# Kernel tuning notes

Hardware: AMD Instinct MI355X
Metric: run time of the kernel (lower is better)

The kernel has to match this reference:

```python
import jax, jax.numpy as jnp
import numpy as np
import math

B, H, W, DM = 4, 64, 64, 96
DS, DCONV, EXPAND = 16, 3, 2
DI = EXPAND * DM
DTR = math.ceil(DM / 16)
K = 4
HID = 4 * DI


def layernorm(x, g, b, eps=1e-5):
    m = x.mean(-1, keepdims=True)
    v = ((x - m) ** 2).mean(-1, keepdims=True)
    return (x - m) / jnp.sqrt(v + eps) * g + b


def dwconv(x, w, b=None):
    # x: (B,C,H,W), w: (C,1,kh,kw) depthwise, odd kernel => SAME padding == k//2
    out = jax.lax.conv_general_dilated(x, w, (1, 1), 'SAME',
                                       feature_group_count=x.shape[1],
                                       dimension_numbers=('NCHW', 'OIHW', 'NCHW'))
    if b is not None:
        out = out + b[None, :, None, None]
    return out


def ss2d_core(xc, x_proj_w, dt_projs_w, dt_projs_b, A_logs, Ds):
    # xc: (b, d_inner, h, w) -> (b, d_inner, L) summed over 4 scan directions
    b, c, h, w = xc.shape
    L = h * w
    x_hw = xc.reshape(b, c, L)
    x_wh = xc.transpose(0, 1, 3, 2).reshape(b, c, L)
    xs = jnp.stack([x_hw, x_wh], axis=1)                 # (b,2,c,L)
    xs = jnp.concatenate([xs, jnp.flip(xs, -1)], axis=1)  # (b,4,c,L)
    x_dbl = jnp.einsum('bkdl,kcd->bkcl', xs, x_proj_w)
    dts, Bs, Cs = jnp.split(x_dbl, [DTR, DTR + DS], axis=2)
    dts = jnp.einsum('bkrl,kdr->bkdl', dts, dt_projs_w)
    delta = jax.nn.softplus(dts + dt_projs_b[None, :, :, None])  # (b,K,c,L)
    A = -jnp.exp(A_logs).reshape(K, c, DS)                       # (K,c,n)

    def step(hst, inp):
        x_t, d_t, B_t, C_t = inp  # (b,K,c),(b,K,c),(b,K,n),(b,K,n)
        dA = jnp.exp(d_t[..., None] * A)                       # (b,K,c,n)
        hst = hst * dA + (d_t * x_t)[..., None] * B_t[:, :, None, :]
        y = jnp.einsum('bkdn,bkn->bkd', hst, C_t)
        return hst, y

    seq = (jnp.moveaxis(xs, -1, 0), jnp.moveaxis(delta, -1, 0),
           jnp.moveaxis(Bs, -1, 0), jnp.moveaxis(Cs, -1, 0))
    h0 = jnp.zeros((b, K, c, DS), xc.dtype)
    _, ys = jax.lax.scan(step, h0, seq)          # (L,b,K,c)
    ys = jnp.moveaxis(ys, 0, -1)                 # (b,K,c,L)
    ys = ys + Ds.reshape(K, c)[None, :, :, None] * xs
    y1 = ys[:, 0]
    inv = jnp.flip(ys[:, 2:4], -1)
    y2 = inv[:, 0]
    wh = ys[:, 1].reshape(b, c, w, h).swapaxes(2, 3).reshape(b, c, L)
    invwh = inv[:, 1].reshape(b, c, w, h).swapaxes(2, 3).reshape(b, c, L)
    return y1 + y2 + wh + invwh


def msffn(y, in_w, in_b, dw1, dw3, dw5, ln_g, ln_b, out_w, out_b):
    hcl = jax.nn.silu(y @ in_w.T + in_b)          # (b,h,w,HID)
    hc = hcl.transpose(0, 3, 1, 2)
    hc = hc + dwconv(hc, dw1) + dwconv(hc, dw3) + dwconv(hc, dw5)
    hn = layernorm(hc.transpose(0, 2, 3, 1), ln_g, ln_b)
    return hn @ out_w.T + out_b


def setup_inputs() -> dict:
    key = jax.random.key(0)
    ks = jax.random.split(key, 16)
    dt_init_std = DTR ** -0.5
    dt = jnp.exp(jax.random.uniform(ks[0], (K, DI)) * (math.log(0.1) - math.log(0.001)) + math.log(0.001))
    dt = jnp.clip(dt, 1e-4, None)
    inv_dt = dt + jnp.log(-jnp.expm1(-dt))          # softplus-inverse init for dt bias
    A_logs = jnp.tile(jnp.log(jnp.arange(1, DS + 1, dtype=jnp.float32))[None, :], (K * DI, 1))
    r = lambda i, sh, s: jax.random.normal(ks[i], sh, jnp.float32) * s
    return {
        'x': r(1, (B, H, W, DM), 1.0),
        'in_proj_w': r(2, (2 * DI, DM), DM ** -0.5),
        'conv_w': r(3, (DI, 1, DCONV, DCONV), 0.2),
        'conv_b': jnp.zeros((DI,), jnp.float32),
        'x_proj_w': r(4, (K, DTR + 2 * DS, DI), DI ** -0.5),
        'dt_projs_w': jax.random.uniform(ks[5], (K, DI, DTR), minval=-dt_init_std, maxval=dt_init_std),
        'dt_projs_b': inv_dt,
        'A_logs': A_logs,
        'Ds': jnp.ones((K * DI,), jnp.float32),
        'out_norm_g': jnp.ones((DI,), jnp.float32),
        'out_norm_b': jnp.zeros((DI,), jnp.float32),
        'out_proj_w': r(6, (DM, DI), DI ** -0.5),
        'ffn_in_w': r(7, (HID, DI), DI ** -0.5),
        'ffn_in_b': jnp.zeros((HID,), jnp.float32),
        'ffn_dw1': r(8, (HID, 1, 1, 1), 0.3),
        'ffn_dw3': r(9, (HID, 1, 3, 3), 0.2),
        'ffn_dw5': r(10, (HID, 1, 5, 5), 0.1),
        'ffn_ln_g': jnp.ones((HID,), jnp.float32),
        'ffn_ln_b': jnp.zeros((HID,), jnp.float32),
        'ffn_out_w': r(11, (DM, HID), HID ** -0.5),
        'ffn_out_b': jnp.zeros((DM,), jnp.float32),
        'skip_scale': jnp.ones((1,), jnp.float32),
    }


def reference(x, in_proj_w, conv_w, conv_b, x_proj_w, dt_projs_w, dt_projs_b, A_logs, Ds,
              out_norm_g, out_norm_b, out_proj_w, ffn_in_w, ffn_in_b, ffn_dw1, ffn_dw3,
              ffn_dw5, ffn_ln_g, ffn_ln_b, ffn_out_w, ffn_out_b, skip_scale):
    b, h, w, _ = x.shape
    xz = x @ in_proj_w.T                          # (b,h,w,2*DI)
    xi, z = jnp.split(xz, 2, axis=-1)
    xc = jax.nn.silu(dwconv(xi.transpose(0, 3, 1, 2), conv_w, conv_b))  # (b,DI,h,w)
    y = ss2d_core(xc, x_proj_w, dt_projs_w, dt_projs_b, A_logs, Ds)     # (b,DI,L)
    y = y.swapaxes(1, 2).reshape(b, h, w, DI)
    y = layernorm(y, out_norm_g, out_norm_b)
    y = y * jax.nn.silu(z)
    out = y @ out_proj_w.T
    ffn = msffn(y, ffn_in_w, ffn_in_b, ffn_dw1, ffn_dw3, ffn_dw5,
                ffn_ln_g, ffn_ln_b, ffn_out_w, ffn_out_b)
    return out + skip_scale * ffn
```

## Files before the change

### kernel.cpp

```cpp
#include <hip/hip_runtime.h>
#include <hip/hip_bf16.h>

constexpr int BB = 4, HH = 64, WW = 64, DMv = 96;
constexpr int DSn = 16, DIv = 192, DTRv = 6, KKv = 4, HIDv = 768;
constexpr int LL = 4096;
constexpr int NC = 64, CHK = LL / NC;
constexpr int NR = BB * LL;
constexpr int XDS = 40;

constexpr size_t S_xi   = (size_t)BB * LL * DIv;
constexpr size_t S_xdbl = (size_t)BB * KKv * LL * XDS;
constexpr size_t S_big  = (size_t)BB * KKv * LL * DIv;
constexpr size_t S_sp   = (size_t)BB * KKv * NC * DIv * DSn;

typedef __attribute__((ext_vector_type(8))) short short8;
typedef __attribute__((ext_vector_type(4))) short short4v;
typedef __attribute__((ext_vector_type(4))) float floatx4;

__device__ __forceinline__ float sigf(float x) { return 1.f / (1.f + __expf(-x)); }
__device__ __forceinline__ float softp(float x) {
  return (x > 20.f) ? x : __logf(1.f + __expf(x));
}
__device__ __forceinline__ short bfbits(float v) {
  __hip_bfloat16 h = __float2bfloat16(v);
  return *(short*)&h;
}

__device__ __forceinline__ int lmap(int k, int l) {
  int lr = (k & 2) ? (LL - 1 - l) : l;
  return (k & 1) ? (((lr & 63) << 6) | (lr >> 6)) : lr;
}

__global__ void k_wprep(const float* __restrict__ fiw, const float* __restrict__ opw,
                        const float* __restrict__ fow, const float* __restrict__ in_w,
                        const float* __restrict__ xpw, const float* __restrict__ x,
                        float* __restrict__ wt, float* __restrict__ xt,
                        short* __restrict__ fiwP, short* __restrict__ opwP,
                        short* __restrict__ fowP, short* __restrict__ wcatP) {
  int bx = blockIdx.x, t = threadIdx.x;
  __shared__ float smbuf[32 * 65];
  if (bx < 36) {
    int r0 = (bx / 3) * 32, c0 = (bx % 3) * 32;
    float (*tile)[33] = (float(*)[33])smbuf;
    int tc = t & 31, tr = t >> 5;
#pragma unroll
    for (int i = 0; i < 4; ++i)
      tile[tr + i * 8][tc] = in_w[(size_t)(r0 + tr + i * 8) * 96 + c0 + tc];
    __syncthreads();
#pragma unroll
    for (int i = 0; i < 4; ++i)
      wt[(size_t)(c0 + tr + i * 8) * 384 + r0 + tc] = tile[tc][tr + i * 8];
    return;
  }
  if (bx < 804) {
    int i4 = bx - 36;
    int r0 = (i4 / 3) * 64, k0 = (i4 % 3) * 32;
    float (*tile)[65] = (float(*)[65])smbuf;
#pragma unroll
    for (int ii = 0; ii < 8; ++ii) {
      int i = (t >> 5) + ii * 8, j = t & 31;
      tile[j][i] = x[(size_t)(r0 + i) * 96 + k0 + j];
    }
    __syncthreads();
#pragma unroll
    for (int jj = 0; jj < 8; ++jj) {
      int j = (t >> 6) + jj * 4, i = t & 63;
      xt[(size_t)(k0 + j) * NR + r0 + i] = tile[j][i];
    }
    return;
  }
  int lane = t & 63, ln16 = lane & 15, qd = lane >> 4;
  if (bx < 876) {
    int f = (bx - 804) * 4 + (t >> 6);
    int kt = f / 48, ntg = f % 48;
    int n = ntg * 16 + ln16;
#pragma unroll
    for (int j = 0; j < 8; ++j) {
      int k = kt * 32 + qd * 8 + j;
      fiwP[(size_t)f * 512 + lane * 8 + j] = bfbits(fiw[(size_t)n * DIv + k]);
    }
    return;
  }
  if (bx < 894) {
    int u = (bx - 876) * 4 + (t >> 6);
    int f = u >> 1, part = u & 1;
    int kt = f / 6, ntg = f % 6;
    int n = ntg * 16 + ln16;
#pragma unroll
    for (int j = 0; j < 8; ++j) {
      int k = kt * 32 + qd * 8 + j;
      float w = opw[(size_t)n * DIv + k];
      __hip_bfloat16 h = __float2bfloat16(w);
      float v = part ? (w - (float)h) : w;
      opwP[((size_t)(part * 36 + f)) * 512 + lane * 8 + j] = bfbits(v);
    }
    return;
  }
  if (bx < 966) {
    int u = (bx - 894) * 4 + (t >> 6);
    int f = u >> 1, part = u & 1;
    int kt = f / 6, ntg = f % 6;
    int n = ntg * 16 + ln16;
#pragma unroll
    for (int j = 0; j < 8; ++j) {
      int k = kt * 32 + qd * 8 + j;
      float w = fow[(size_t)n * HIDv + k];
      __hip_bfloat16 h = __float2bfloat16(w);
      float v = part ? (w - (float)h) : w;
      fowP[((size_t)(part * 144 + f)) * 512 + lane * 8 + j] = bfbits(v);
    }
    return;
  }
  {
    int u = (bx - 966) * 4 + (t >> 6);
    int p = u / 60, r = u % 60;
    int part = r / 30, r2 = r % 30;
    int kt = r2 / 5, g = r2 % 5;
    int n = g * 16 + ln16;
#pragma unroll
    for (int j = 0; j < 8; ++j) {
      int kd = kt * 32 + qd * 8 + j;
      float w = 0.f;
      if (n < 76) {
        int ksel = ((n >= 38) ? 2 : 0) + p;
        int cc = (n >= 38) ? n - 38 : n;
        w = xpw[(size_t)(ksel * 38 + cc) * DIv + kd];
      }
      __hip_bfloat16 h = __float2bfloat16(w);
      float v = part ? (w - (float)h) : w;
      wcatP[((size_t)(((p * 2 + part) * 6 + kt) * 5 + g)) * 512 + lane * 8 + j] = bfbits(v);
    }
  }
}

__global__ void k_inproj(const float* __restrict__ xt, const float* __restrict__ wt,
                         float* __restrict__ xi, float* __restrict__ z) {
  int t = threadIdx.x;
  int wv = t >> 6, lane = t & 63;
  int rq = blockIdx.x * 256 + wv * 64 + lane;
  int c0 = blockIdx.y * 8;
  const float4* xt4 = (const float4*)xt;
  float4 acc[8];
#pragma unroll
  for (int c = 0; c < 8; ++c) acc[c] = make_float4(0.f, 0.f, 0.f, 0.f);
  for (int k = 0; k < 96; ++k) {
    float4 xv = xt4[(size_t)k * (NR / 4) + rq];
    const float* wr = wt + k * 384 + c0;
#pragma unroll
    for (int c = 0; c < 8; ++c) {
      float w = wr[c];
      acc[c].x += w * xv.x; acc[c].y += w * xv.y;
      acc[c].z += w * xv.z; acc[c].w += w * xv.w;
    }
  }
  float* dst; int cc;
  if (c0 < DIv) { dst = xi; cc = c0; } else { dst = z; cc = c0 - DIv; }
#pragma unroll
  for (int li = 0; li < 4; ++li) {
    size_t row = (size_t)rq * 4 + li;
    float4 v0, v1;
    v0.x = (&acc[0].x)[li]; v0.y = (&acc[1].x)[li];
    v0.z = (&acc[2].x)[li]; v0.w = (&acc[3].x)[li];
    v1.x = (&acc[4].x)[li]; v1.y = (&acc[5].x)[li];
    v1.z = (&acc[6].x)[li]; v1.w = (&acc[7].x)[li];
    float4* o4 = (float4*)(dst + row * DIv + cc);
    o4[0] = v0; o4[1] = v1;
  }
}

constexpr int TW2 = 18;
__global__ void k_dwconv3(const float* __restrict__ xi, const float* __restrict__ cw,
                          const float* __restrict__ cb, float* __restrict__ xc,
                          short* __restrict__ xcBh, short* __restrict__ xcBl) {
  int tile = blockIdx.x;
  int cg = blockIdx.y, b = blockIdx.z;
  int t = threadIdx.x;
  int ti0 = (tile >> 2) * 16, tj0 = (tile & 3) * 16;
  __shared__ float sm[TW2 * TW2 * 32];

  for (int e = t; e < TW2 * TW2 * 32; e += 256) {
    int ec = e & 31;
    int sp = e >> 5;
    int hi = sp / TW2, hj = sp % TW2;
    int gi = ti0 + hi - 1, gj = tj0 + hj - 1;
    float v = 0.f;
    if ((unsigned)gi < (unsigned)HH && (unsigned)gj < (unsigned)WW)
      v = xi[((size_t)b * LL + gi * WW + gj) * DIv + cg * 32 + ec];
    sm[e] = v;
  }

  int c = t & 31, s0 = t >> 5;
  int cglob = cg * 32 + c;
  float wc[9];
#pragma unroll
  for (int j = 0; j < 9; ++j) wc[j] = cw[cglob * 9 + j];
  float bv = cb[cglob];
  __syncthreads();

  float res[32];
  for (int i = 0; i < 32; ++i) {
    int p = s0 + (i << 3);
    int r = p >> 4, q = p & 15;
    float s = bv;
#pragma unroll
    for (int di = 0; di < 3; ++di)
#pragma unroll
      for (int dj = 0; dj < 3; ++dj)
        s += sm[((r + di) * TW2 + (q + dj)) * 32 + c] * wc[di * 3 + dj];
    res[i] = s * sigf(s);
  }
  __syncthreads();
  for (int i = 0; i < 32; ++i) {
    int p = s0 + (i << 3);
    sm[p * 35 + c] = res[i];
  }
  __syncthreads();
  for (int it = 0; it < 32; ++it) {
    int e = it * 256 + t;
    int p = e >> 5, ec = e & 31;
    int l = (ti0 + (p >> 4)) * WW + tj0 + (p & 15);
    float v = sm[p * 35 + ec];
    size_t idx = ((size_t)b * LL + l) * DIv + cg * 32 + ec;
    xc[idx] = v;
    __hip_bfloat16 hh = __float2bfloat16(v);
    xcBh[idx] = *(short*)&hh;
    xcBl[idx] = bfbits(v - (float)hh);
  }
}

__global__ void k_xdblmf(const short* __restrict__ xcBh, const short* __restrict__ xcBl,
                         const short* __restrict__ wcatP, float* __restrict__ xdbl) {
  int t = threadIdx.x;
  int wv = t >> 6, lane = t & 63;
  int ln16 = lane & 15, qd = lane >> 4;
  int pb = blockIdx.y;
  int p = pb >> 2, b = pb & 3;
  int m0 = blockIdx.x * 64 + wv * 16;
  int r = m0 + ln16;
  int l = p ? (((r & 63) << 6) | (r >> 6)) : r;
  const short* ah = xcBh + ((size_t)(b * LL + l)) * DIv + qd * 8;
  const short* al = xcBl + ((size_t)(b * LL + l)) * DIv + qd * 8;
  floatx4 acc[5];
  floatx4 zero4 = {0.f, 0.f, 0.f, 0.f};
#pragma unroll
  for (int g = 0; g < 5; ++g) acc[g] = zero4;
#pragma unroll
  for (int kt = 0; kt < 6; ++kt) {
    short8 Ah = *(const short8*)(ah + kt * 32);
    short8 Al = *(const short8*)(al + kt * 32);
    const short* bh = wcatP + ((size_t)(((p * 2 + 0) * 6 + kt) * 5)) * 512 + lane * 8;
    const short* bl = wcatP + ((size_t)(((p * 2 + 1) * 6 + kt) * 5)) * 512 + lane * 8;
#pragma unroll
    for (int g = 0; g < 5; ++g) {
      short8 Bh = *(const short8*)(bh + (size_t)g * 512);
      short8 Bl = *(const short8*)(bl + (size_t)g * 512);
      acc[g] = __builtin_amdgcn_mfma_f32_16x16x32_bf16(Ah, Bh, acc[g], 0, 0, 0);
      acc[g] = __builtin_amdgcn_mfma_f32_16x16x32_bf16(Al, Bh, acc[g], 0, 0, 0);
      acc[g] = __builtin_amdgcn_mfma_f32_16x16x32_bf16(Ah, Bl, acc[g], 0, 0, 0);
    }
  }
#pragma unroll
  for (int g = 0; g < 5; ++g) {
    int col = g * 16 + ln16;
    if (col < 76) {
#pragma unroll
      for (int rr = 0; rr < 4; ++rr) {
        int rowr = m0 + qd * 4 + rr;
        int kk = (col >= 38) ? (2 + p) : p;
        int cc = (col >= 38) ? col - 38 : col;
        int lpos = (col >= 38) ? (LL - 1 - rowr) : rowr;
        int phys = cc + (cc >= 6 ? 2 : 0);
        size_t ro = (((size_t)(b * KKv + kk)) * LL + lpos) * XDS;
        xdbl[ro + phys] = acc[g][rr];
        if (col == 5) { xdbl[ro + 6] = 0.f; xdbl[ro + 7] = 0.f; }
      }
    }
  }
}

__global__ void k_scan1(const float* __restrict__ xdbl, const float* __restrict__ xc,
                        const float* __restrict__ alogs, const float* __restrict__ dtw,
                        const float* __restrict__ dtb,
                        float* __restrict__ S, float* __restrict__ P) {
  int bx = blockIdx.x;
  int c = bx / 3, dblk = bx % 3;
  int k = blockIdx.y, b = blockIdx.z;
  int t = threadIdx.x, dl = t >> 2, nq = t & 3;
  int d = dblk * 64 + dl;
  __shared__ float de_s[16][64], xv_s[16][64], bc_s[16][16];
  float A[4];
#pragma unroll
  for (int j = 0; j < 4; ++j)
    A[j] = -__expf(alogs[(size_t)(k * DIv + d) * DSn + nq * 4 + j]);
  int derow = t >> 4, dec0 = (t & 15) * 4;
  float DTW[4][6], DTB[4];
#pragma unroll
  for (int jj = 0; jj < 4; ++jj) {
    int dd = k * DIv + dblk * 64 + dec0 + jj;
    DTB[jj] = dtb[dd];
#pragma unroll
    for (int r2 = 0; r2 < 6; ++r2) DTW[jj][r2] = dtw[(size_t)dd * 6 + r2];
  }
  size_t bkL = (size_t)(b * KKv + k) * LL;
  const float* xq = xdbl + bkL * XDS;
  const float* xcb = xc + (size_t)b * LL * DIv;
  float h[4] = {0.f, 0.f, 0.f, 0.f}, sA[4] = {0.f, 0.f, 0.f, 0.f};
  int l0 = c * CHK;
  for (int tile = 0; tile < CHK / 16; ++tile) {
    int lt = l0 + tile * 16;
    __syncthreads();
    {
      int r = t >> 4, q = t & 15;
      int lc = lmap(k, lt + r);
      *(float4*)&xv_s[r][q * 4] = *(const float4*)(xcb + (size_t)lc * DIv + dblk * 64 + q * 4);
      if (t < 64) {
        int r2 = t >> 2, q2 = t & 3;
        *(float4*)&bc_s[r2][q2 * 4] = *(const float4*)(xq + (size_t)(lt + r2) * XDS + 8 + q2 * 4);
      }
      const float* dtp = xq + (size_t)(lt + derow) * XDS;
      float d0 = dtp[0], d1 = dtp[1], d2 = dtp[2], d3 = dtp[3], d4 = dtp[4], d5 = dtp[5];
#pragma unroll
      for (int jj = 0; jj < 4; ++jj) {
        float s = DTB[jj] + d0 * DTW[jj][0] + d1 * DTW[jj][1] + d2 * DTW[jj][2]
                          + d3 * DTW[jj][3] + d4 * DTW[jj][4] + d5 * DTW[jj][5];
        de_s[derow][dec0 + jj] = softp(s);
      }
    }
    __syncthreads();
#pragma unroll
    for (int i2 = 0; i2 < 16; ++i2) {
      float de = de_s[i2][dl];
      float xv = xv_s[i2][dl];
      float4 Bv = *(float4*)&bc_s[i2][nq * 4];
      float db = de * xv;
#pragma unroll
      for (int j = 0; j < 4; ++j) {
        float u = de * A[j];
        sA[j] += u;
        h[j] = h[j] * __expf(u) + db * (&Bv.x)[j];
      }
    }
  }
  size_t o = ((((size_t)(b * KKv + k) * NC + c) * 3 + dblk) * 1024) + (size_t)t * 4;
  float4 hs, ps;
#pragma unroll
  for (int j = 0; j < 4; ++j) { (&hs.x)[j] = h[j]; (&ps.x)[j] = __expf(sA[j]); }
  *(float4*)(S + o) = hs;
  *(float4*)(P + o) = ps;
}

__global__ void k_scan2(float* __restrict__ S, const float* __restrict__ P) {
  int dblk = blockIdx.x, k = blockIdx.y, b = blockIdx.z;
  int t = threadIdx.x;
  size_t base = (((size_t)(b * KKv + k) * NC) * 3 + dblk) * 1024 + (size_t)t * 4;
  float4 h = make_float4(0.f, 0.f, 0.f, 0.f);
  for (int c = 0; c < NC; ++c) {
    size_t o = base + (size_t)c * 3 * 1024;
    float4 s = *(float4*)(S + o), p = *(float4*)(P + o);
    *(float4*)(S + o) = h;
    h.x = s.x + p.x * h.x; h.y = s.y + p.y * h.y;
    h.z = s.z + p.z * h.z; h.w = s.w + p.w * h.w;
  }
}

__global__ void k_scan3(const float* __restrict__ xdbl, const float* __restrict__ xc,
                        const float* __restrict__ alogs, const float* __restrict__ dtw,
                        const float* __restrict__ dtb,
                        const float* __restrict__ Hin, float* __restrict__ ys) {
  int bx = blockIdx.x;
  int c = bx / 3, dblk = bx % 3;
  int k = blockIdx.y, b = blockIdx.z;
  int t = threadIdx.x, dl = t >> 2, nq = t & 3;
  int d = dblk * 64 + dl;
  __shared__ float de_s[16][64], xv_s[16][64], bc_s[16][32];
  float A[4];
#pragma unroll
  for (int j = 0; j < 4; ++j)
    A[j] = -__expf(alogs[(size_t)(k * DIv + d) * DSn + nq * 4 + j]);
  int derow = t >> 4, dec0 = (t & 15) * 4;
  float DTW[4][6], DTB[4];
#pragma unroll
  for (int jj = 0; jj < 4; ++jj) {
    int dd = k * DIv + dblk * 64 + dec0 + jj;
    DTB[jj] = dtb[dd];
#pragma unroll
    for (int r2 = 0; r2 < 6; ++r2) DTW[jj][r2] = dtw[(size_t)dd * 6 + r2];
  }
  size_t bkL = (size_t)(b * KKv + k) * LL;
  const float* xq = xdbl + bkL * XDS;
  const float* xcb = xc + (size_t)b * LL * DIv;
  float* yp = ys + bkL * DIv + d;
  size_t o = ((((size_t)(b * KKv + k) * NC + c) * 3 + dblk) * 1024) + (size_t)t * 4;
  float4 h4 = *(const float4*)(Hin + o);
  float h[4] = {h4.x, h4.y, h4.z, h4.w};
  int l0 = c * CHK;
  for (int tile = 0; tile < CHK / 16; ++tile) {
    int lt = l0 + tile * 16;
    __syncthreads();
    {
      int r = t >> 4, q = t & 15;
      int lc = lmap(k, lt + r);
      *(float4*)&xv_s[r][q * 4] = *(const float4*)(xcb + (size_t)lc * DIv + dblk * 64 + q * 4);
      if (t < 128) {
        int r2 = t >> 3, q2 = t & 7;
        *(float4*)&bc_s[r2][q2 * 4] = *(const float4*)(xq + (size_t)(lt + r2) * XDS + 8 + q2 * 4);
      }
      const float* dtp = xq + (size_t)(lt + derow) * XDS;
      float d0 = dtp[0], d1 = dtp[1], d2 = dtp[2], d3 = dtp[3], d4 = dtp[4], d5 = dtp[5];
#pragma unroll
      for (int jj = 0; jj < 4; ++jj) {
        float s = DTB[jj] + d0 * DTW[jj][0] + d1 * DTW[jj][1] + d2 * DTW[jj][2]
                          + d3 * DTW[jj][3] + d4 * DTW[jj][4] + d5 * DTW[jj][5];
        de_s[derow][dec0 + jj] = softp(s);
      }
    }
    __syncthreads();
#pragma unroll
    for (int i2 = 0; i2 < 16; ++i2) {
      float de = de_s[i2][dl];
      float xv = xv_s[i2][dl];
      float4 Bv = *(float4*)&bc_s[i2][nq * 4];
      float4 Cv = *(float4*)&bc_s[i2][16 + nq * 4];
      float db = de * xv;
      float p = 0.f;
#pragma unroll
      for (int j = 0; j < 4; ++j) {
        h[j] = h[j] * __expf(de * A[j]) + db * (&Bv.x)[j];
        p += h[j] * (&Cv.x)[j];
      }
      p += __shfl_down(p, 2, 4);
      p += __shfl_down(p, 1, 4);
      if (nq == 0) yp[(size_t)(lt + i2) * DIv] = p;
    }
  }
}

__global__ void k_comlnt(const float* __restrict__ ys, const float* __restrict__ xc,
                         const float* __restrict__ Ds, const float* __restrict__ z,
                         const float* __restrict__ g, const float* __restrict__ be,
                         __hip_bfloat16* __restrict__ ygtB,
                         __hip_bfloat16* __restrict__ ygtBl) {
  int bl0 = blockIdx.x * 8;
  int b = bl0 >> 12, l0 = bl0 & 4095;
  int t = threadIdx.x;
  __shared__ float vbuf[8 * 193];
  __shared__ float m_[8], rs_[8];
  {
    int li = t >> 5, lane32 = t & 31;
    size_t base = (size_t)b * KKv * LL * DIv;
    int l = l0 + li;
    int lT = ((l & 63) << 6) | (l >> 6);
    const float* r0 = ys + base + (size_t)l * DIv;
    const float* r2 = ys + base + ((size_t)2 * LL + (LL - 1 - l)) * DIv;
    const float* r1 = ys + base + ((size_t)1 * LL + lT) * DIv;
    const float* r3 = ys + base + ((size_t)3 * LL + (LL - 1 - lT)) * DIv;
    const float* xr = xc + ((size_t)b * LL + l) * DIv;
#pragma unroll
    for (int cc = 0; cc < 6; ++cc) {
      int d = lane32 + cc * 32;
      float sd = Ds[d] + Ds[DIv + d] + Ds[2 * DIv + d] + Ds[3 * DIv + d];
      vbuf[li * 193 + d] = r0[d] + r2[d] + r1[d] + r3[d] + sd * xr[d];
    }
  }
  __syncthreads();
  {
    int r = t >> 5, q = t & 31;
    float s = 0.f, qq = 0.f;
#pragma unroll
    for (int j = 0; j < 6; ++j) {
      float v = vbuf[r * 193 + q + j * 32];
      s += v; qq += v * v;
    }
    s += __shfl_down(s, 16, 32); qq += __shfl_down(qq, 16, 32);
    s += __shfl_down(s, 8, 32);  qq += __shfl_down(qq, 8, 32);
    s += __shfl_down(s, 4, 32);  qq += __shfl_down(qq, 4, 32);
    s += __shfl_down(s, 2, 32);  qq += __shfl_down(qq, 2, 32);
    s += __shfl_down(s, 1, 32);  qq += __shfl_down(qq, 1, 32);
    if (q == 0) {
      float m = s / DIv;
      m_[r] = m;
      rs_[r] = rsqrtf(qq / DIv - m * m + 1e-5f);
    }
  }
  __syncthreads();
  int tc = t & 31, tr = t >> 5;
#pragma unroll
  for (int ch = 0; ch < 6; ++ch) {
    int c0 = ch * 32;
    float gg = g[c0 + tc], bb = be[c0 + tc];
    float v = vbuf[tr * 193 + c0 + tc];
    float zz = z[(size_t)(bl0 + tr) * DIv + c0 + tc];
    float val = (v - m_[tr]) * rs_[tr] * gg + bb;
    float gated = val * zz * sigf(zz);
    __hip_bfloat16 h = __float2bfloat16(gated);
    ygtB[(size_t)(bl0 + tr) * DIv + c0 + tc] = h;
    ygtBl[(size_t)(bl0 + tr) * DIv + c0 + tc] = __float2bfloat16(gated - (float)h);
  }
}

__global__ void k_ffnmf(const __hip_bfloat16* __restrict__ ygtB,
                        const short* __restrict__ fiwP,
                        const float* __restrict__ bias, float* __restrict__ hcl) {
  int t = threadIdx.x;
  int wv = t >> 6, lane = t & 63;
  int ln16 = lane & 15, qd = lane >> 4;
  int m0 = blockIdx.x * 64 + wv * 16;
  int n0 = blockIdx.y * 64;
  int ntg0 = n0 >> 4;
  floatx4 acc[4];
  floatx4 zero4 = {0.f, 0.f, 0.f, 0.f};
#pragma unroll
  for (int nt = 0; nt < 4; ++nt) acc[nt] = zero4;
  const short* arow = (const short*)ygtB + (size_t)(m0 + ln16) * DIv + qd * 8;
#pragma unroll
  for (int kt = 0; kt < 6; ++kt) {
    short8 a = *(const short8*)(arow + kt * 32);
    const short* bb = fiwP + ((size_t)(kt * 48 + ntg0) * 64 + lane) * 8;
#pragma unroll
    for (int nt = 0; nt < 4; ++nt) {
      short8 bfr = *(const short8*)(bb + (size_t)nt * 512);
      acc[nt] = __builtin_amdgcn_mfma_f32_16x16x32_bf16(a, bfr, acc[nt], 0, 0, 0);
    }
  }
#pragma unroll
  for (int nt = 0; nt < 4; ++nt) {
    int col = n0 + nt * 16 + ln16;
    float bv = bias[col];
#pragma unroll
    for (int r = 0; r < 4; ++r) {
      int row = m0 + qd * 4 + r;
      float s = acc[nt][r] + bv;
      hcl[(size_t)row * HIDv + col] = s * sigf(s);
    }
  }
}

constexpr int TS = 16, CG = 16, TW = TS + 4;
__global__ void k_ffnconv2(const float* __restrict__ hcl, const float* __restrict__ w1,
                           const float* __restrict__ w3, const float* __restrict__ w5,
                           float* __restrict__ hc2) {
  int tile = blockIdx.x;
  int cg = blockIdx.y, b = blockIdx.z;
  int t = threadIdx.x;
  int ti0 = (tile >> 2) * TS, tj0 = (tile & 3) * TS;
  __shared__ float sm[TW * TW * CG];

  for (int e = t; e < TW * TW * CG; e += 256) {
    int ec = e & 15;
    int sp = e >> 4;
    int hi = sp / TW, hj = sp % TW;
    int gi = ti0 + hi - 2, gj = tj0 + hj - 2;
    float v = 0.f;
    if ((unsigned)gi < (unsigned)HH && (unsigned)gj < (unsigned)WW)
      v = hcl[((size_t)b * LL + gi * WW + gj) * HIDv + cg * CG + ec];
    sm[e] = v;
  }

  int c = t & 15;
  int q = t >> 4;
  int cglob = cg * CG + c;
  float wc[25];
#pragma unroll
  for (int di = 0; di < 5; ++di)
#pragma unroll
    for (int dj = 0; dj < 5; ++dj) {
      float w = w5[cglob * 25 + di * 5 + dj];
      if (di >= 1 && di <= 3 && dj >= 1 && dj <= 3)
        w += w3[cglob * 9 + (di - 1) * 3 + (dj - 1)];
      if (di == 2 && dj == 2) w += 1.f + w1[cglob];
      wc[di * 5 + dj] = w;
    }
  __syncthreads();

  float win[5][5];
#pragma unroll
  for (int di = 0; di < 4; ++di)
#pragma unroll
    for (int dj = 0; dj < 5; ++dj)
      win[di][dj] = sm[(di * TW + (q + dj)) * CG + c];
#pragma unroll
  for (int r = 0; r < 16; ++r) {
    int slot = (r + 4) % 5;
#pragma unroll
    for (int dj = 0; dj < 5; ++dj)
      win[slot][dj] = sm[(((r + 4) * TW) + (q + dj)) * CG + c];
    float s = 0.f;
#pragma unroll
    for (int di = 0; di < 5; ++di) {
      int wsl = (r + di) % 5;
#pragma unroll
      for (int dj = 0; dj < 5; ++dj)
        s += win[wsl][dj] * wc[di * 5 + dj];
    }
    hc2[((size_t)b * LL + (ti0 + r) * WW + (tj0 + q)) * HIDv + cglob] = s;
  }
}

constexpr int LNROWS = 8, LNPAD = 776;
__global__ void k_ln2b(const float* __restrict__ hc2, const float* __restrict__ g,
                       const float* __restrict__ be,
                       short* __restrict__ hnBh, short* __restrict__ hnBl) {
  int r0 = blockIdx.x * LNROWS;
  int t = threadIdx.x;
  __shared__ float rows[LNROWS * LNPAD];
  __shared__ float m_[LNROWS], rs_[LNROWS];
#pragma unroll
  for (int i = 0; i < 6; ++i) {
    int idx4 = t + i * 256;
    int row = idx4 / 192, c4 = idx4 % 192;
    float4 v = *(const float4*)(hc2 + (size_t)(r0 + row) * HIDv + c4 * 4);
    *(float4*)&rows[row * LNPAD + c4 * 4] = v;
  }
  __syncthreads();
  {
    int r = t >> 5, q = t & 31;
    float s = 0.f, qq = 0.f;
#pragma unroll
    for (int j = 0; j < 24; ++j) {
      float v = rows[r * LNPAD + q + j * 32];
      s += v; qq += v * v;
    }
    s += __shfl_down(s, 16, 32); qq += __shfl_down(qq, 16, 32);
    s += __shfl_down(s, 8, 32);  qq += __shfl_down(qq, 8, 32);
    s += __shfl_down(s, 4, 32);  qq += __shfl_down(qq, 4, 32);
    s += __shfl_down(s, 2, 32);  qq += __shfl_down(qq, 2, 32);
    s += __shfl_down(s, 1, 32);  qq += __shfl_down(qq, 1, 32);
    if (q == 0) {
      float m = s / HIDv;
      m_[r] = m;
      rs_[r] = rsqrtf(qq / HIDv - m * m + 1e-5f);
    }
  }
  __syncthreads();
#pragma unroll
  for (int i = 0; i < 6; ++i) {
    int idx4 = t + i * 256;
    int row = idx4 / 192, c4 = idx4 % 192;
    float4 v = *(const float4*)&rows[row * LNPAD + c4 * 4];
    float4 gv = *(const float4*)(g + c4 * 4);
    float4 bv = *(const float4*)(be + c4 * 4);
    float m = m_[row], rs = rs_[row];
    short4v hh, ll;
#pragma unroll
    for (int j = 0; j < 4; ++j) {
      float val = ((&v.x)[j] - m) * rs * (&gv.x)[j] + (&bv.x)[j];
      __hip_bfloat16 h = __float2bfloat16(val);
      hh[j] = *(short*)&h;
      ll[j] = bfbits(val - (float)h);
    }
    size_t o = (size_t)(r0 + row) * HIDv + c4 * 4;
    *(short4v*)(hnBh + o) = hh;
    *(short4v*)(hnBl + o) = ll;
  }
}

__global__ void k_finalmf(const short* __restrict__ hnBh, const short* __restrict__ hnBl,
                          const short* __restrict__ fowP,
                          const short* __restrict__ ygtBh, const short* __restrict__ ygtBl,
                          const short* __restrict__ opwP,
                          const float* __restrict__ fob, const float* __restrict__ skip,
                          float* __restrict__ part) {
  int t = threadIdx.x;
  int wv = t >> 6, lane = t & 63;
  int ln16 = lane & 15, qd = lane >> 4;
  int m0 = blockIdx.x * 64 + wv * 16;
  int ks = blockIdx.y;
  floatx4 accF[6];
  floatx4 zero4 = {0.f, 0.f, 0.f, 0.f};
#pragma unroll
  for (int nt = 0; nt < 6; ++nt) accF[nt] = zero4;
  const short* arh = hnBh + (size_t)(m0 + ln16) * HIDv + qd * 8;
  const short* arl = hnBl + (size_t)(m0 + ln16) * HIDv + qd * 8;
  int kt0 = ks * 12;
#pragma unroll 2
  for (int kt = kt0; kt < kt0 + 12; ++kt) {
    short8 ah = *(const short8*)(arh + kt * 32);
    short8 al = *(const short8*)(arl + kt * 32);
    const short* bh = fowP + ((size_t)(kt * 6) * 64 + lane) * 8;
    const short* bl = fowP + ((size_t)(144 + kt * 6) * 64 + lane) * 8;
#pragma unroll
    for (int nt = 0; nt < 6; ++nt) {
      short8 bhv = *(const short8*)(bh + (size_t)nt * 512);
      short8 blv = *(const short8*)(bl + (size_t)nt * 512);
      accF[nt] = __builtin_amdgcn_mfma_f32_16x16x32_bf16(ah, bhv, accF[nt], 0, 0, 0);
      accF[nt] = __builtin_amdgcn_mfma_f32_16x16x32_bf16(al, bhv, accF[nt], 0, 0, 0);
      accF[nt] = __builtin_amdgcn_mfma_f32_16x16x32_bf16(ah, blv, accF[nt], 0, 0, 0);
    }
  }
  float sk = skip[0];
  if (ks == 0) {
    floatx4 accO[6];
#pragma unroll
    for (int nt = 0; nt < 6; ++nt) accO[nt] = zero4;
    const short* orh = ygtBh + (size_t)(m0 + ln16) * DIv + qd * 8;
    const short* orl = ygtBl + (size_t)(m0 + ln16) * DIv + qd * 8;
#pragma unroll 2
    for (int kt = 0; kt < 6; ++kt) {
      short8 ah = *(const short8*)(orh + kt * 32);
      short8 al = *(const short8*)(orl + kt * 32);
      const short* bh = opwP + ((size_t)(kt * 6) * 64 + lane) * 8;
      const short* bl = opwP + ((size_t)(36 + kt * 6) * 64 + lane) * 8;
#pragma unroll
      for (int nt = 0; nt < 6; ++nt) {
        short8 bhv = *(const short8*)(bh + (size_t)nt * 512);
        short8 blv = *(const short8*)(bl + (size_t)nt * 512);
        accO[nt] = __builtin_amdgcn_mfma_f32_16x16x32_bf16(ah, bhv, accO[nt], 0, 0, 0);
        accO[nt] = __builtin_amdgcn_mfma_f32_16x16x32_bf16(al, bhv, accO[nt], 0, 0, 0);
        accO[nt] = __builtin_amdgcn_mfma_f32_16x16x32_bf16(ah, blv, accO[nt], 0, 0, 0);
      }
    }
#pragma unroll
    for (int nt = 0; nt < 6; ++nt) {
      int col = nt * 16 + ln16;
#pragma unroll
      for (int r = 0; r < 4; ++r) {
        int row = m0 + qd * 4 + r;
        part[(size_t)row * DMv + col] = accO[nt][r] + sk * accF[nt][r];
      }
    }
  } else {
#pragma unroll
    for (int nt = 0; nt < 6; ++nt) {
      int col = nt * 16 + ln16;
      float bv = fob[col];
#pragma unroll
      for (int r = 0; r < 4; ++r) {
        int row = m0 + qd * 4 + r;
        part[(size_t)NR * DMv + (size_t)row * DMv + col] = sk * (accF[nt][r] + bv);
      }
    }
  }
}

__global__ void k_finmerge(const float* __restrict__ part, float* __restrict__ dout) {
  size_t i = (size_t)blockIdx.x * 256 + threadIdx.x;
  const float4* p4 = (const float4*)part;
  size_t npart = (size_t)NR * DMv / 4;
  float4 a = p4[i], b = p4[i + npart];
  float4 r;
  r.x = a.x + b.x; r.y = a.y + b.y; r.z = a.z + b.z; r.w = a.w + b.w;
  ((float4*)dout)[i] = r;
}

extern "C" void kernel_launch(void* const* d_in, const int* in_sizes, int n_in,
                              void* d_out, int out_size, void* d_ws, size_t ws_size,
                              hipStream_t stream) {
  const float* x        = (const float*)d_in[0];
  const float* in_w     = (const float*)d_in[1];
  const float* conv_w   = (const float*)d_in[2];
  const float* conv_b   = (const float*)d_in[3];
  const float* xpw      = (const float*)d_in[4];
  const float* dtw      = (const float*)d_in[5];
  const float* dtb      = (const float*)d_in[6];
  const float* alogs    = (const float*)d_in[7];
  const float* Ds       = (const float*)d_in[8];
  const float* ong      = (const float*)d_in[9];
  const float* onb      = (const float*)d_in[10];
  const float* opw      = (const float*)d_in[11];
  const float* fiw      = (const float*)d_in[12];
  const float* fib      = (const float*)d_in[13];
  const float* dw1      = (const float*)d_in[14];
  const float* dw3      = (const float*)d_in[15];
  const float* dw5      = (const float*)d_in[16];
  const float* flg      = (const float*)d_in[17];
  const float* flb      = (const float*)d_in[18];
  const float* fow      = (const float*)d_in[19];
  const float* fob      = (const float*)d_in[20];
  const float* skip     = (const float*)d_in[21];

  float* ws    = (float*)d_ws;
  float* xi    = ws;
  float* z     = xi + S_xi;
  float* xc    = z + S_xi;
  float* xdbl  = xc + S_xi;
  float* scr   = xdbl + S_xdbl;
  float* ys    = scr + S_big;
  float* wtiny = ys + S_big;
  float* wt    = wtiny;
  __hip_bfloat16* ygtB = (__hip_bfloat16*)(wt + 36864);
  short* fiwP  = (short*)(wt + 36864) + (size_t)NR * DIv;
  short* opwP  = fiwP + 288 * 512;
  short* fowP  = opwP + 2 * 36 * 512;
  short* wcatP = fowP + 2 * 144 * 512;

  float* xt = scr;
  k_wprep<<<996, 256, 0, stream>>>(fiw, opw, fow, in_w, xpw, x,
                                   wt, xt, fiwP, opwP, fowP, wcatP);

  dim3 gip(NR / 1024, 48);
  k_inproj<<<gip, 256, 0, stream>>>(xt, wt, xi, z);

  short* xcBh = (short*)ys;
  short* xcBl = xcBh + (size_t)NR * DIv;
  dim3 gdw(16, DIv / 32, BB);
  k_dwconv3<<<gdw, 256, 0, stream>>>(xi, conv_w, conv_b, xc, xcBh, xcBl);

  dim3 gxd(LL / 64, 8);
  k_xdblmf<<<gxd, 256, 0, stream>>>(xcBh, xcBl, wcatP, xdbl);

  float* Sbuf = scr;
  float* Pbuf = scr + S_sp;
  dim3 gs13(NC * 3, KKv, BB);
  dim3 gs2(3, KKv, BB);
  k_scan1<<<gs13, 256, 0, stream>>>(xdbl, xc, alogs, dtw, dtb, Sbuf, Pbuf);
  k_scan2<<<gs2, 256, 0, stream>>>(Sbuf, Pbuf);
  k_scan3<<<gs13, 256, 0, stream>>>(xdbl, xc, alogs, dtw, dtb, Sbuf, ys);

  __hip_bfloat16* ygtBl = (__hip_bfloat16*)xi;
  k_comlnt<<<NR / 8, 256, 0, stream>>>(ys, xc, Ds, z, ong, onb, ygtB, ygtBl);

  float* hcl = scr;
  dim3 gmf(NR / 64, HIDv / 64);
  k_ffnmf<<<gmf, 256, 0, stream>>>(ygtB, fiwP, fib, hcl);

  float* hc2 = ys;
  dim3 gc(16, HIDv / CG, BB);
  k_ffnconv2<<<gc, 256, 0, stream>>>(hcl, dw1, dw3, dw5, hc2);

  short* hnBh = (short*)scr;
  short* hnBl = hnBh + (size_t)NR * HIDv;
  k_ln2b<<<NR / LNROWS, 256, 0, stream>>>(hc2, flg, flb, hnBh, hnBl);

  float* partbuf = z;
  dim3 gfm(NR / 64, 2);
  k_finalmf<<<gfm, 256, 0, stream>>>(hnBh, hnBl, fowP,
                                     (const short*)ygtB, (const short*)ygtBl, opwP,
                                     fob, skip, partbuf);
  k_finmerge<<<(NR * DMv / 4) / 256, 256, 0, stream>>>(partbuf, (float*)d_out);
}
```

Measured before the change: 393.6 us.

## Move input projection to split-bf16 MFMA and double scan tile length

The scalar fp32 input projection, which used a transposed copy of x, is replaced by an MFMA kernel. x is split into bf16 high and low parts, and three bf16 MFMAs per tile approximate fp32 accuracy. The weight prep now packs in_proj weights into MFMA fragment layout and converts x directly, so the transpose pass is dropped. Separately, the scan1 and scan3 kernels stage 32 timesteps per shared-memory tile instead of 16, which halves the barriers per chunk at the cost of more shared memory.

```diff
diff --git a/kernel.cpp b/kernel.cpp
--- a/kernel.cpp
+++ b/kernel.cpp
@@ -34,44 +34,48 @@
 __global__ void k_wprep(const float* __restrict__ fiw, const float* __restrict__ opw,
                         const float* __restrict__ fow, const float* __restrict__ in_w,
                         const float* __restrict__ xpw, const float* __restrict__ x,
-                        float* __restrict__ wt, float* __restrict__ xt,
-                        short* __restrict__ fiwP, short* __restrict__ opwP,
-                        short* __restrict__ fowP, short* __restrict__ wcatP) {
+                        short* __restrict__ xBh, short* __restrict__ xBl,
+                        short* __restrict__ inwP, short* __restrict__ fiwP,
+                        short* __restrict__ opwP, short* __restrict__ fowP,
+                        short* __restrict__ wcatP) {
   int bx = blockIdx.x, t = threadIdx.x;
-  __shared__ float smbuf[32 * 65];
-  if (bx < 36) {
-    int r0 = (bx / 3) * 32, c0 = (bx % 3) * 32;
-    float (*tile)[33] = (float(*)[33])smbuf;
-    int tc = t & 31, tr = t >> 5;
-#pragma unroll
-    for (int i = 0; i < 4; ++i)
-      tile[tr + i * 8][tc] = in_w[(size_t)(r0 + tr + i * 8) * 96 + c0 + tc];
-    __syncthreads();
-#pragma unroll
-    for (int i = 0; i < 4; ++i)
-      wt[(size_t)(c0 + tr + i * 8) * 384 + r0 + tc] = tile[tc][tr + i * 8];
+  if (bx < 384) {
+    const float4* x4 = (const float4*)x;
+#pragma unroll
+    for (int i = 0; i < 4; ++i) {
+      int idx4 = bx * 1024 + i * 256 + t;
+      float4 v = x4[idx4];
+      short4v hh, ll;
+#pragma unroll
+      for (int j = 0; j < 4; ++j) {
+        float val = (&v.x)[j];
+        __hip_bfloat16 h = __float2bfloat16(val);
+        hh[j] = *(short*)&h;
+        ll[j] = bfbits(val - (float)h);
+      }
+      *(short4v*)(xBh + (size_t)idx4 * 4) = hh;
+      *(short4v*)(xBl + (size_t)idx4 * 4) = ll;
+    }
     return;
   }
-  if (bx < 804) {
-    int i4 = bx - 36;
-    int r0 = (i4 / 3) * 64, k0 = (i4 % 3) * 32;
-    float (*tile)[65] = (float(*)[65])smbuf;
-#pragma unroll
-    for (int ii = 0; ii < 8; ++ii) {
-      int i = (t >> 5) + ii * 8, j = t & 31;
-      tile[j][i] = x[(size_t)(r0 + i) * 96 + k0 + j];
-    }
-    __syncthreads();
-#pragma unroll
-    for (int jj = 0; jj < 8; ++jj) {
-      int j = (t >> 6) + jj * 4, i = t & 63;
-      xt[(size_t)(k0 + j) * NR + r0 + i] = tile[j][i];
+  int lane = t & 63, ln16 = lane & 15, qd = lane >> 4;
+  if (bx < 420) {
+    int u = (bx - 384) * 4 + (t >> 6);
+    int f = u >> 1, part = u & 1;
+    int kt = f / 24, ntg = f % 24;
+    int n = ntg * 16 + ln16;
+#pragma unroll
+    for (int j = 0; j < 8; ++j) {
+      int k = kt * 32 + qd * 8 + j;
+      float w = in_w[(size_t)n * 96 + k];
+      __hip_bfloat16 h = __float2bfloat16(w);
+      float v = part ? (w - (float)h) : w;
+      inwP[((size_t)(part * 72 + f)) * 512 + lane * 8 + j] = bfbits(v);
     }
     return;
   }
-  int lane = t & 63, ln16 = lane & 15, qd = lane >> 4;
-  if (bx < 876) {
-    int f = (bx - 804) * 4 + (t >> 6);
+  if (bx < 492) {
+    int f = (bx - 420) * 4 + (t >> 6);
     int kt = f / 48, ntg = f % 48;
     int n = ntg * 16 + ln16;
 #pragma unroll
@@ -81,8 +85,8 @@
     }
     return;
   }
-  if (bx < 894) {
-    int u = (bx - 876) * 4 + (t >> 6);
+  if (bx < 510) {
+    int u = (bx - 492) * 4 + (t >> 6);
     int f = u >> 1, part = u & 1;
     int kt = f / 6, ntg = f % 6;
     int n = ntg * 16 + ln16;
@@ -96,8 +100,8 @@
     }
     return;
   }
-  if (bx < 966) {
-    int u = (bx - 894) * 4 + (t >> 6);
+  if (bx < 582) {
+    int u = (bx - 510) * 4 + (t >> 6);
     int f = u >> 1, part = u & 1;
     int kt = f / 6, ntg = f % 6;
     int n = ntg * 16 + ln16;
@@ -112,7 +116,7 @@
     return;
   }
   {
-    int u = (bx - 966) * 4 + (t >> 6);
+    int u = (bx - 582) * 4 + (t >> 6);
     int p = u / 60, r = u % 60;
     int part = r / 30, r2 = r % 30;
     int kt = r2 / 5, g = r2 % 5;
@@ -133,38 +137,45 @@
   }
 }
 
-__global__ void k_inproj(const float* __restrict__ xt, const float* __restrict__ wt,
-                         float* __restrict__ xi, float* __restrict__ z) {
+__global__ void k_inprojmf(const short* __restrict__ xBh, const short* __restrict__ xBl,
+                           const short* __restrict__ inwP,
+                           float* __restrict__ xi, float* __restrict__ z) {
   int t = threadIdx.x;
   int wv = t >> 6, lane = t & 63;
-  int rq = blockIdx.x * 256 + wv * 64 + lane;
-  int c0 = blockIdx.y * 8;
-  const float4* xt4 = (const float4*)xt;
-  float4 acc[8];
-#pragma unroll
-  for (int c = 0; c < 8; ++c) acc[c] = make_float4(0.f, 0.f, 0.f, 0.f);
-  for (int k = 0; k < 96; ++k) {
-    float4 xv = xt4[(size_t)k * (NR / 4) + rq];
-    const float* wr = wt + k * 384 + c0;
-#pragma unroll
-    for (int c = 0; c < 8; ++c) {
-      float w = wr[c];
-      acc[c].x += w * xv.x; acc[c].y += w * xv.y;
-      acc[c].z += w * xv.z; acc[c].w += w * xv.w;
-    }
-  }
-  float* dst; int cc;
-  if (c0 < DIv) { dst = xi; cc = c0; } else { dst = z; cc = c0 - DIv; }
-#pragma unroll
-  for (int li = 0; li < 4; ++li) {
-    size_t row = (size_t)rq * 4 + li;
-    float4 v0, v1;
-    v0.x = (&acc[0].x)[li]; v0.y = (&acc[1].x)[li];
-    v0.z = (&acc[2].x)[li]; v0.w = (&acc[3].x)[li];
-    v1.x = (&acc[4].x)[li]; v1.y = (&acc[5].x)[li];
-    v1.z = (&acc[6].x)[li]; v1.w = (&acc[7].x)[li];
-    float4* o4 = (float4*)(dst + row * DIv + cc);
-    o4[0] = v0; o4[1] = v1;
+  int ln16 = lane & 15, qd = lane >> 4;
+  int m0 = blockIdx.x * 64 + wv * 16;
+  int ntg0 = blockIdx.y * 4;
+  floatx4 acc[4];
+  floatx4 zero4 = {0.f, 0.f, 0.f, 0.f};
+#pragma unroll
+  for (int nt = 0; nt < 4; ++nt) acc[nt] = zero4;
+  const short* arh = xBh + (size_t)(m0 + ln16) * 96 + qd * 8;
+  const short* arl = xBl + (size_t)(m0 + ln16) * 96 + qd * 8;
+#pragma unroll
+  for (int kt = 0; kt < 3; ++kt) {
+    short8 ah = *(const short8*)(arh + kt * 32);
+    short8 al = *(const short8*)(arl + kt * 32);
+    const short* bh = inwP + ((size_t)(kt * 24 + ntg0) * 64 + lane) * 8;
+    const short* bl = inwP + ((size_t)(72 + kt * 24 + ntg0) * 64 + lane) * 8;
+#pragma unroll
+    for (int nt = 0; nt < 4; ++nt) {
+      short8 Bh = *(const short8*)(bh + (size_t)nt * 512);
+      short8 Bl = *(const short8*)(bl + (size_t)nt * 512);
+      acc[nt] = __builtin_amdgcn_mfma_f32_16x16x32_bf16(ah, Bh, acc[nt], 0, 0, 0);
+      acc[nt] = __builtin_amdgcn_mfma_f32_16x16x32_bf16(al, Bh, acc[nt], 0, 0, 0);
+      acc[nt] = __builtin_amdgcn_mfma_f32_16x16x32_bf16(ah, Bl, acc[nt], 0, 0, 0);
+    }
+  }
+#pragma unroll
+  for (int nt = 0; nt < 4; ++nt) {
+    int col = blockIdx.y * 64 + nt * 16 + ln16;
+#pragma unroll
+    for (int r = 0; r < 4; ++r) {
+      int row = m0 + qd * 4 + r;
+      float v = acc[nt][r];
+      if (col < DIv) xi[(size_t)row * DIv + col] = v;
+      else           z[(size_t)row * DIv + col - DIv] = v;
+    }
   }
 }
 
@@ -287,7 +298,7 @@
   int k = blockIdx.y, b = blockIdx.z;
   int t = threadIdx.x, dl = t >> 2, nq = t & 3;
   int d = dblk * 64 + dl;
-  __shared__ float de_s[16][64], xv_s[16][64], bc_s[16][16];
+  __shared__ float de_s[32][64], xv_s[32][64], bc_s[32][16];
   float A[4];
 #pragma unroll
   for (int j = 0; j < 4; ++j)
@@ -306,29 +317,37 @@
   const float* xcb = xc + (size_t)b * LL * DIv;
   float h[4] = {0.f, 0.f, 0.f, 0.f}, sA[4] = {0.f, 0.f, 0.f, 0.f};
   int l0 = c * CHK;
-  for (int tile = 0; tile < CHK / 16; ++tile) {
-    int lt = l0 + tile * 16;
+  for (int tile = 0; tile < CHK / 32; ++tile) {
+    int lt = l0 + tile * 32;
     __syncthreads();
     {
       int r = t >> 4, q = t & 15;
-      int lc = lmap(k, lt + r);
-      *(float4*)&xv_s[r][q * 4] = *(const float4*)(xcb + (size_t)lc * DIv + dblk * 64 + q * 4);
-      if (t < 64) {
+#pragma unroll
+      for (int rr = 0; rr < 2; ++rr) {
+        int row = r + rr * 16;
+        int lc = lmap(k, lt + row);
+        *(float4*)&xv_s[row][q * 4] = *(const float4*)(xcb + (size_t)lc * DIv + dblk * 64 + q * 4);
+      }
+      if (t < 128) {
         int r2 = t >> 2, q2 = t & 3;
         *(float4*)&bc_s[r2][q2 * 4] = *(const float4*)(xq + (size_t)(lt + r2) * XDS + 8 + q2 * 4);
       }
-      const float* dtp = xq + (size_t)(lt + derow) * XDS;
-      float d0 = dtp[0], d1 = dtp[1], d2 = dtp[2], d3 = dtp[3], d4 = dtp[4], d5 = dtp[5];
-#pragma unroll
-      for (int jj = 0; jj < 4; ++jj) {
-        float s = DTB[jj] + d0 * DTW[jj][0] + d1 * DTW[jj][1] + d2 * DTW[jj][2]
-                          + d3 * DTW[jj][3] + d4 * DTW[jj][4] + d5 * DTW[jj][5];
-        de_s[derow][dec0 + jj] = softp(s);
+#pragma unroll
+      for (int rr = 0; rr < 2; ++rr) {
+        int row = derow + rr * 16;
+        const float* dtp = xq + (size_t)(lt + row) * XDS;
+        float d0 = dtp[0], d1 = dtp[1], d2 = dtp[2], d3 = dtp[3], d4 = dtp[4], d5 = dtp[5];
+#pragma unroll
+        for (int jj = 0; jj < 4; ++jj) {
+          float s = DTB[jj] + d0 * DTW[jj][0] + d1 * DTW[jj][1] + d2 * DTW[jj][2]
+                            + d3 * DTW[jj][3] + d4 * DTW[jj][4] + d5 * DTW[jj][5];
+          de_s[row][dec0 + jj] = softp(s);
+        }
       }
     }
     __syncthreads();
 #pragma unroll
-    for (int i2 = 0; i2 < 16; ++i2) {
+    for (int i2 = 0; i2 < 32; ++i2) {
       float de = de_s[i2][dl];
       float xv = xv_s[i2][dl];
       float4 Bv = *(float4*)&bc_s[i2][nq * 4];
@@ -372,7 +391,7 @@
   int k = blockIdx.y, b = blockIdx.z;
   int t = threadIdx.x, dl = t >> 2, nq = t & 3;
   int d = dblk * 64 + dl;
-  __shared__ float de_s[16][64], xv_s[16][64], bc_s[16][32];
+  __shared__ float de_s[32][64], xv_s[32][64], bc_s[32][32];
   float A[4];
 #pragma unroll
   for (int j = 0; j < 4; ++j)
@@ -394,29 +413,37 @@
   float4 h4 = *(const float4*)(Hin + o);
   float h[4] = {h4.x, h4.y, h4.z, h4.w};
   int l0 = c * CHK;
-  for (int tile = 0; tile < CHK / 16; ++tile) {
-    int lt = l0 + tile * 16;
+  for (int tile = 0; tile < CHK / 32; ++tile) {
+    int lt = l0 + tile * 32;
     __syncthreads();
     {
       int r = t >> 4, q = t & 15;
-      int lc = lmap(k, lt + r);
-      *(float4*)&xv_s[r][q * 4] = *(const float4*)(xcb + (size_t)lc * DIv + dblk * 64 + q * 4);
-      if (t < 128) {
+#pragma unroll
+      for (int rr = 0; rr < 2; ++rr) {
+        int row = r + rr * 16;
+        int lc = lmap(k, lt + row);
+        *(float4*)&xv_s[row][q * 4] = *(const float4*)(xcb + (size_t)lc * DIv + dblk * 64 + q * 4);
+      }
+      {
         int r2 = t >> 3, q2 = t & 7;
         *(float4*)&bc_s[r2][q2 * 4] = *(const float4*)(xq + (size_t)(lt + r2) * XDS + 8 + q2 * 4);
       }
-      const float* dtp = xq + (size_t)(lt + derow) * XDS;
-      float d0 = dtp[0], d1 = dtp[1], d2 = dtp[2], d3 = dtp[3], d4 = dtp[4], d5 = dtp[5];
-#pragma unroll
-      for (int jj = 0; jj < 4; ++jj) {
-        float s = DTB[jj] + d0 * DTW[jj][0] + d1 * DTW[jj][1] + d2 * DTW[jj][2]
-                          + d3 * DTW[jj][3] + d4 * DTW[jj][4] + d5 * DTW[jj][5];
-        de_s[derow][dec0 + jj] = softp(s);
+#pragma unroll
+      for (int rr = 0; rr < 2; ++rr) {
+        int row = derow + rr * 16;
+        const float* dtp = xq + (size_t)(lt + row) * XDS;
+        float d0 = dtp[0], d1 = dtp[1], d2 = dtp[2], d3 = dtp[3], d4 = dtp[4], d5 = dtp[5];
+#pragma unroll
+        for (int jj = 0; jj < 4; ++jj) {
+          float s = DTB[jj] + d0 * DTW[jj][0] + d1 * DTW[jj][1] + d2 * DTW[jj][2]
+                            + d3 * DTW[jj][3] + d4 * DTW[jj][4] + d5 * DTW[jj][5];
+          de_s[row][dec0 + jj] = softp(s);
+        }
       }
     }
     __syncthreads();
 #pragma unroll
-    for (int i2 = 0; i2 < 16; ++i2) {
+    for (int i2 = 0; i2 < 32; ++i2) {
       float de = de_s[i2][dl];
       float xv = xv_s[i2][dl];
       float4 Bv = *(float4*)&bc_s[i2][nq * 4];
@@ -776,19 +803,20 @@
   float* scr   = xdbl + S_xdbl;
   float* ys    = scr + S_big;
   float* wtiny = ys + S_big;
-  float* wt    = wtiny;
-  __hip_bfloat16* ygtB = (__hip_bfloat16*)(wt + 36864);
-  short* fiwP  = (short*)(wt + 36864) + (size_t)NR * DIv;
+  short* inwP  = (short*)wtiny;
+  __hip_bfloat16* ygtB = (__hip_bfloat16*)(wtiny + 36864);
+  short* fiwP  = (short*)(wtiny + 36864) + (size_t)NR * DIv;
   short* opwP  = fiwP + 288 * 512;
   short* fowP  = opwP + 2 * 36 * 512;
   short* wcatP = fowP + 2 * 144 * 512;
 
-  float* xt = scr;
-  k_wprep<<<996, 256, 0, stream>>>(fiw, opw, fow, in_w, xpw, x,
-                                   wt, xt, fiwP, opwP, fowP, wcatP);
-
-  dim3 gip(NR / 1024, 48);
-  k_inproj<<<gip, 256, 0, stream>>>(xt, wt, xi, z);
+  short* xBh = (short*)scr;
+  short* xBl = xBh + (size_t)NR * 96;
+  k_wprep<<<612, 256, 0, stream>>>(fiw, opw, fow, in_w, xpw, x,
+                                   xBh, xBl, inwP, fiwP, opwP, fowP, wcatP);
+
+  dim3 gipm(NR / 64, 6);
+  k_inprojmf<<<gipm, 256, 0, stream>>>(xBh, xBl, inwP, xi, z);
 
   short* xcBh = (short*)ys;
   short* xcBl = xcBh + (size_t)NR * DIv;
```

After: 599.3 us. +52.3%, slower.
